# Performance work log

Hardware: AMD Instinct MI355X
Metric: run time of the kernel (lower is better)

Reference implementation:

```python
import jax, jax.numpy as jnp
import numpy as np
import math

DIM = 1024
ATTN_DIM = 1024
B, S = 2, 4096

def setup_inputs() -> dict:
    key = jax.random.key(0)
    k1, k2, k3 = jax.random.split(key, 3)
    x = jax.random.normal(k1, (B, S, DIM), dtype=jnp.float32)
    # qkv Linear(dim, 3*attn_dim, bias=True): weight [3*attn_dim, dim], bias [3*attn_dim]
    W_qkv = jax.random.normal(k2, (3 * ATTN_DIM, DIM), dtype=jnp.float32) * (1.0 / math.sqrt(DIM))
    b_qkv = jax.random.normal(k3, (3 * ATTN_DIM,), dtype=jnp.float32) * 0.01
    return {"x": x, "W_qkv": W_qkv, "b_qkv": b_qkv}

def reference(x, W_qkv, b_qkv):
    b, s, d = x.shape
    qkv = jnp.einsum('bsd,ed->bse', x, W_qkv) + b_qkv  # [B,S,3*attn_dim]
    q, k, v = jnp.split(qkv, 3, axis=-1)
    score = jnp.einsum('bqd,bkd->bqk', q, k)  # [B,S,S]
    # causal mask applied BEFORE scaling (matches original: -inf survives the divide)
    causal = jnp.tril(jnp.ones((s, s), dtype=bool))
    score = jnp.where(causal, score, -jnp.inf)
    attn = jax.nn.softmax(score / math.sqrt(ATTN_DIM), axis=-1)
    y = jnp.einsum('bqk,bkd->bqd', attn, v)  # [B,S,attn_dim]
    return y
```

## Files before the change

### kernel.cpp

```cpp
#include <hip/hip_runtime.h>
#include <cstdint>
#include <cstddef>

typedef __bf16 bf16;
typedef bf16 bf16x4 __attribute__((ext_vector_type(4)));
typedef bf16 bf16x8 __attribute__((ext_vector_type(8)));
typedef float f32x4 __attribute__((ext_vector_type(4)));

#define SEQ 4096
#define DIMD 1024
#define TILE_K1024 131072L
#define TILE_K4096 524288L
#define PC_BATCH   8650752L

__device__ __forceinline__ void async16(void* lds, const void* g) {
    __builtin_amdgcn_global_load_lds(
        (__attribute__((address_space(1))) void*)g,
        (__attribute__((address_space(3))) void*)lds,
        16, 0, 0);
}

__device__ __forceinline__ void gemm_core(
    const bf16* __restrict__ At, const bf16* __restrict__ Bt,
    int k0, int k1, f32x4 acc[4][4])
{
    __shared__ bf16 lA[4096];
    __shared__ bf16 lB[4096];
    const int tid  = threadIdx.x;
    const int lane = tid & 63;
    const int wid  = tid >> 6;
    const int wm   = (wid >> 1) * 64;
    const int wn   = (wid & 1) * 64;
    const int lr   = lane & 15;
    const int kq   = (lane >> 4) * 8;

    for (int kk = k0; kk < k1; ++kk) {
        const bf16* sa = At + (long)kk * 4096;
        const bf16* sb = Bt + (long)kk * 4096;
        async16(&lA[tid * 8],        sa + tid * 8);
        async16(&lA[2048 + tid * 8], sa + 2048 + tid * 8);
        async16(&lB[tid * 8],        sb + tid * 8);
        async16(&lB[2048 + tid * 8], sb + 2048 + tid * 8);
        __syncthreads();

        bf16x8 af[4], bfr[4];
#pragma unroll
        for (int mi = 0; mi < 4; ++mi)
            af[mi] = *(const bf16x8*)&lA[(wm + mi * 16 + lr) * 32 + kq];
#pragma unroll
        for (int ni = 0; ni < 4; ++ni)
            bfr[ni] = *(const bf16x8*)&lB[(wn + ni * 16 + lr) * 32 + kq];
#pragma unroll
        for (int mi = 0; mi < 4; ++mi)
#pragma unroll
            for (int ni = 0; ni < 4; ++ni)
                acc[mi][ni] = __builtin_amdgcn_mfma_f32_16x16x32_bf16(
                    af[mi], bfr[ni], acc[mi][ni], 0, 0, 0);
        __syncthreads();
    }
}

__global__ __launch_bounds__(256) void cvt_all_kernel(
    const float* __restrict__ x, const float* __restrict__ W,
    bf16* __restrict__ xt, bf16* __restrict__ wt, float* __restrict__ sums)
{
    const int g = blockIdx.x, tid = threadIdx.x;
    if (g >= 11264) { sums[(g - 11264) * 256 + tid] = 0.0f; return; }
    const float* in; bf16* out; int i;
    if (g < 8192) { in = x; out = xt; i = g * 256 + tid; }
    else          { in = W; out = wt; i = (g - 8192) * 256 + tid; }
    const float4 v = ((const float4*)in)[i];
    const int j = i * 4, row = j >> 10, col = j & 1023;
    const long o = (long)(row >> 7) * TILE_K1024 + (col >> 5) * 4096
                 + (row & 127) * 32 + (col & 31);
    bf16x4 ov = { (bf16)v.x, (bf16)v.y, (bf16)v.z, (bf16)v.w };
    *(bf16x4*)&out[o] = ov;
}

__global__ __launch_bounds__(256) void qkv_gemm(
    const bf16* __restrict__ xt, const bf16* __restrict__ wt,
    const float* __restrict__ bias,
    bf16* __restrict__ Qt, bf16* __restrict__ Kt, bf16* __restrict__ Vtt)
{
    const int b = blockIdx.x, x = b & 7, r = b >> 3;
    const int mt = x * 8 + r / 24, wnid = r % 24;
    const int bm = mt * 128, bn = wnid * 128;

    f32x4 acc[4][4] = {};
    gemm_core(xt + (long)mt * TILE_K1024, wt + (long)wnid * TILE_K1024, 0, 32, acc);

    const int tid = threadIdx.x, lane = tid & 63, wid = tid >> 6;
    const int wm = (wid >> 1) * 64, wn = (wid & 1) * 64;
    const int lr = lane & 15, q4 = (lane >> 4) * 4;
#pragma unroll
    for (int ni = 0; ni < 4; ++ni) {
        const int n = bn + wn + ni * 16 + lr;
        const float bv = bias[n];
#pragma unroll
        for (int mi = 0; mi < 4; ++mi) {
            const int m0 = bm + wm + mi * 16 + q4;
            if (n < 2048) {
                bf16* dst = (n < 1024) ? Qt : Kt;
                const int c = n & 1023;
#pragma unroll
                for (int rr = 0; rr < 4; ++rr) {
                    const int m = m0 + rr;
                    dst[(long)(m >> 7) * TILE_K1024 + (c >> 5) * 4096
                        + (m & 127) * 32 + (c & 31)] = (bf16)(acc[mi][ni][rr] + bv);
                }
            } else {
                const int bb = m0 >> 12, s = m0 & 4095, d = n - 2048;
                bf16x4 o = { (bf16)(acc[mi][ni][0] + bv), (bf16)(acc[mi][ni][1] + bv),
                             (bf16)(acc[mi][ni][2] + bv), (bf16)(acc[mi][ni][3] + bv) };
                *(bf16x4*)&Vtt[(long)bb * 4194304 + (long)(d >> 7) * TILE_K4096
                               + (s >> 5) * 4096 + (d & 127) * 32 + (s & 31)] = o;
            }
        }
    }
}

__global__ __launch_bounds__(256) void score_kernel(
    const bf16* __restrict__ Qt, const bf16* __restrict__ Kt,
    bf16* __restrict__ Pc, float* __restrict__ sums)
{
    const int b = blockIdx.x, x = b & 7;
    int r = b >> 3;
    const int bz = r / 66, batch = bz;
    r %= 66;
    int qt, kt;
    const int s0 = x + 1;
    if (r < s0)           { qt = x;      kt = r; }
    else if (r < 33)      { qt = 31 - x; kt = r - s0; }
    else if (r < 42 + x)  { qt = x + 8;  kt = r - 33; }
    else                  { qt = 23 - x; kt = r - 42 - x; }

    bf16* Pb = Pc + (long)bz * PC_BATCH + (long)(qt * (qt + 1) / 2 + kt) * 16384;
    float* sb = sums + (long)batch * SEQ;

    f32x4 acc[4][4] = {};
    gemm_core(Qt + (long)(batch * 32 + qt) * TILE_K1024,
              Kt + (long)(batch * 32 + kt) * TILE_K1024, 0, 32, acc);

    const int tid = threadIdx.x, lane = tid & 63, wid = tid >> 6;
    const int wm = (wid >> 1) * 64, wn = (wid & 1) * 64;
    const int lr = lane & 15, q4 = (lane >> 4) * 4;
#pragma unroll
    for (int mi = 0; mi < 4; ++mi) {
#pragma unroll
        for (int rr = 0; rr < 4; ++rr) {
            const int ql = wm + mi * 16 + q4 + rr;
            const int q  = qt * 128 + ql;
            float rsum = 0.0f;
#pragma unroll
            for (int ni = 0; ni < 4; ++ni) {
                const int kl  = wn + ni * 16 + lr;
                const int key = kt * 128 + kl;
                const float s = acc[mi][ni][rr] * 0.03125f;
                const float p = (key <= q) ? __expf(s) : 0.0f;
                const bf16 pb = (bf16)p;
                Pb[(kl >> 5) * 4096 + ql * 32 + (kl & 31)] = pb;
                rsum += (float)pb;
            }
            rsum += __shfl_xor(rsum, 1);
            rsum += __shfl_xor(rsum, 2);
            rsum += __shfl_xor(rsum, 4);
            rsum += __shfl_xor(rsum, 8);
            if (lr == 0) atomicAdd(&sb[q], rsum);
        }
    }
}

__device__ const unsigned char pv_sched[96] = {
     15, 125,  28,  44,  25,  54,  86,  51,  83, 112,   4,   3,
     47,  93,  60,  12,  57,  22, 118,  19, 115,  80,  36,  35,
     31,  61,  92, 122,  89, 119,  10,  41,  18,  48,   5,   2,
     63,  29, 124,  90, 121,  87,  42,   9,  50,  16,  37,  34,
     95,  46,  13,  58,  24,  55,  21, 116,  82, 113,   7,   0,
    127,  14,  45,  26,  56,  23,  53,  84, 114,  81,  39,  32,
     30, 126,  27, 123,  88,  43,  85,  52,   8,  49,   6,   1,
     62,  94,  59,  91, 120,  11, 117,  20,  40,  17,  38,  33,
};

__global__ __launch_bounds__(256) void pv_kernel(
    const bf16* __restrict__ Pc, const bf16* __restrict__ Vtt,
    const float* __restrict__ sums, float* __restrict__ Y,
    float* __restrict__ part)
{
    const int b = blockIdx.x, x = b & 7, t = b >> 3;
    const int j = t >> 3, dt = t & 7;
    const int e = pv_sched[x * 12 + j];
    const int qt = e & 31, bz = (e >> 5) & 1, c = e >> 6;
    const int full = (qt + 1) * 4, half = (qt + 1) * 2;
    int k0, k1;
    if (qt < 16) { k0 = 0; k1 = full; }
    else { k0 = c ? half : 0; k1 = c ? full : half; }
    const int batch = bz;

    f32x4 acc[4][4] = {};
    gemm_core(Pc + (long)bz * PC_BATCH + (long)(qt * (qt + 1) / 2) * 16384,
              Vtt + (long)batch * 4194304 + (long)dt * TILE_K4096, k0, k1, acc);

    const int tid = threadIdx.x, lane = tid & 63, wid = tid >> 6;
    const int wm = (wid >> 1) * 64, wn = (wid & 1) * 64;
    const int lr = lane & 15, q4 = (lane >> 4) * 4;
#pragma unroll
    for (int mi = 0; mi < 4; ++mi) {
#pragma unroll
        for (int rr = 0; rr < 4; ++rr) {
            const int q = qt * 128 + wm + mi * 16 + q4 + rr;
            const float iv = 1.0f / sums[(long)batch * SEQ + q];
#pragma unroll
            for (int ni = 0; ni < 4; ++ni) {
                const int d = dt * 128 + wn + ni * 16 + lr;
                const float v = acc[mi][ni][rr] * iv;
                if (c == 0)
                    Y[(long)batch * 4194304 + (long)q * DIMD + d] = v;
                else
                    part[(long)bz * 2097152 + (long)(q - 2048) * DIMD + d] = v;
            }
        }
    }
}

__global__ __launch_bounds__(256) void combine_kernel(
    float* __restrict__ Y, const float* __restrict__ part)
{
    const long g = (long)blockIdx.x * 256 + threadIdx.x;
    const long e4 = g * 4;
    const int bz = (int)(e4 >> 21);
    const long rem = e4 & 2097151;
    float4 a = *(const float4*)&Y[(long)bz * 4194304 + 2097152 + rem];
    const float4 p = *(const float4*)&part[e4];
    a.x += p.x; a.y += p.y; a.z += p.z; a.w += p.w;
    *(float4*)&Y[(long)bz * 4194304 + 2097152 + rem] = a;
}

extern "C" void kernel_launch(void* const* d_in, const int* in_sizes, int n_in,
                              void* d_out, int out_size, void* d_ws, size_t ws_size,
                              hipStream_t stream)
{
    const float* x    = (const float*)d_in[0];
    const float* W    = (const float*)d_in[1];
    const float* bqkv = (const float*)d_in[2];
    float* out = (float*)d_out;
    char* ws = (char*)d_ws;

    bf16* Pc   = (bf16*)ws;
    bf16* xt   = (bf16*)ws;
    bf16* wt   = (bf16*)(ws + 16 * 1024 * 1024);
    bf16* Kt   = (bf16*)(ws + 34603008);
    bf16* Vtt  = (bf16*)(ws + 51380224);
    float* sums = (float*)(ws + 68157440);
    bf16* Qt   = (bf16*)d_out;
    float* part = (float*)Kt;

    cvt_all_kernel<<<11296, 256, 0, stream>>>(x, W, xt, wt, sums);
    qkv_gemm<<<1536, 256, 0, stream>>>(xt, wt, bqkv, Qt, Kt, Vtt);
    score_kernel<<<1056, 256, 0, stream>>>(Qt, Kt, Pc, sums);
    pv_kernel<<<768, 256, 0, stream>>>(Pc, Vtt, sums, out, part);
    combine_kernel<<<4096, 256, 0, stream>>>(out, part);
}
```

Baseline: 275.2 us.

## Swizzle tiled bf16 layout and load A operand directly from global

```diff
diff --git a/kernel.cpp b/kernel.cpp
--- a/kernel.cpp
+++ b/kernel.cpp
@@ -13,6 +13,10 @@
 #define TILE_K4096 524288L
 #define PC_BATCH   8650752L
 
+__device__ __forceinline__ int swz(int r, int c) {
+    return r * 32 + (((((c >> 3) ^ (r >> 1)) & 3)) << 3) + (c & 7);
+}
+
 __device__ __forceinline__ void async16(void* lds, const void* g) {
     __builtin_amdgcn_global_load_lds(
         (__attribute__((address_space(1))) void*)g,
@@ -24,7 +28,6 @@
     const bf16* __restrict__ At, const bf16* __restrict__ Bt,
     int k0, int k1, f32x4 acc[4][4])
 {
-    __shared__ bf16 lA[4096];
     __shared__ bf16 lB[4096];
     const int tid  = threadIdx.x;
     const int lane = tid & 63;
@@ -32,24 +35,35 @@
     const int wm   = (wid >> 1) * 64;
     const int wn   = (wid & 1) * 64;
     const int lr   = lane & 15;
-    const int kq   = (lane >> 4) * 8;
+    const int q    = lane >> 4;
+
+    int offA[4], offB[4];
+#pragma unroll
+    for (int mi = 0; mi < 4; ++mi) {
+        const int rA = wm + mi * 16 + lr;
+        offA[mi] = rA * 32 + ((((rA >> 1) ^ q) & 3) << 3);
+    }
+#pragma unroll
+    for (int ni = 0; ni < 4; ++ni) {
+        const int rB = wn + ni * 16 + lr;
+        offB[ni] = rB * 32 + ((((rB >> 1) ^ q) & 3) << 3);
+    }
 
     for (int kk = k0; kk < k1; ++kk) {
         const bf16* sa = At + (long)kk * 4096;
         const bf16* sb = Bt + (long)kk * 4096;
-        async16(&lA[tid * 8],        sa + tid * 8);
-        async16(&lA[2048 + tid * 8], sa + 2048 + tid * 8);
+        bf16x8 af[4];
+#pragma unroll
+        for (int mi = 0; mi < 4; ++mi)
+            af[mi] = *(const bf16x8*)(sa + offA[mi]);
         async16(&lB[tid * 8],        sb + tid * 8);
         async16(&lB[2048 + tid * 8], sb + 2048 + tid * 8);
         __syncthreads();
 
-        bf16x8 af[4], bfr[4];
-#pragma unroll
-        for (int mi = 0; mi < 4; ++mi)
-            af[mi] = *(const bf16x8*)&lA[(wm + mi * 16 + lr) * 32 + kq];
+        bf16x8 bfr[4];
 #pragma unroll
         for (int ni = 0; ni < 4; ++ni)
-            bfr[ni] = *(const bf16x8*)&lB[(wn + ni * 16 + lr) * 32 + kq];
+            bfr[ni] = *(const bf16x8*)&lB[offB[ni]];
 #pragma unroll
         for (int mi = 0; mi < 4; ++mi)
 #pragma unroll
@@ -72,7 +86,7 @@
     const float4 v = ((const float4*)in)[i];
     const int j = i * 4, row = j >> 10, col = j & 1023;
     const long o = (long)(row >> 7) * TILE_K1024 + (col >> 5) * 4096
-                 + (row & 127) * 32 + (col & 31);
+                 + swz(row & 127, col & 31);
     bf16x4 ov = { (bf16)v.x, (bf16)v.y, (bf16)v.z, (bf16)v.w };
     *(bf16x4*)&out[o] = ov;
 }
@@ -106,14 +120,14 @@
                 for (int rr = 0; rr < 4; ++rr) {
                     const int m = m0 + rr;
                     dst[(long)(m >> 7) * TILE_K1024 + (c >> 5) * 4096
-                        + (m & 127) * 32 + (c & 31)] = (bf16)(acc[mi][ni][rr] + bv);
+                        + swz(m & 127, c & 31)] = (bf16)(acc[mi][ni][rr] + bv);
                 }
             } else {
                 const int bb = m0 >> 12, s = m0 & 4095, d = n - 2048;
                 bf16x4 o = { (bf16)(acc[mi][ni][0] + bv), (bf16)(acc[mi][ni][1] + bv),
                              (bf16)(acc[mi][ni][2] + bv), (bf16)(acc[mi][ni][3] + bv) };
                 *(bf16x4*)&Vtt[(long)bb * 4194304 + (long)(d >> 7) * TILE_K4096
-                               + (s >> 5) * 4096 + (d & 127) * 32 + (s & 31)] = o;
+                               + (s >> 5) * 4096 + swz(d & 127, s & 31)] = o;
             }
         }
     }
@@ -158,7 +172,7 @@
                 const float s = acc[mi][ni][rr] * 0.03125f;
                 const float p = (key <= q) ? __expf(s) : 0.0f;
                 const bf16 pb = (bf16)p;
-                Pb[(kl >> 5) * 4096 + ql * 32 + (kl & 31)] = pb;
+                Pb[(kl >> 5) * 4096 + swz(ql, kl & 31)] = pb;
                 rsum += (float)pb;
             }
             rsum += __shfl_xor(rsum, 1);
```

Measured after the change: 266.9 us. 3.0% less time.
